# Kernel optimization log

Hardware: AMD Instinct MI355X
Metric: run time of the kernel (lower is better)

The kernel has to match this reference:

```python
import jax, jax.numpy as jnp
import numpy as np

NUM_HEADS = 8
SCALE = 3
TOPKS = [16, 8, 8]  # index 0 = coarsest level


def avg_pool2(t):
    B, C, H, W = t.shape
    return t.reshape(B, C, H // 2, 2, W // 2, 2).mean(axis=(3, 5))


def _to_heads(t, Hi, Wi):
    # [B, C, Hi, Wi] with C = nh*hd (head-major channels) -> [B, nh, Hi*Wi, hd]
    B, C = t.shape[0], t.shape[1]
    hd = C // NUM_HEADS
    return t.reshape(B, NUM_HEADS, hd, Hi * Wi).transpose(0, 1, 3, 2)


def setup_inputs() -> dict:
    key = jax.random.key(0)
    ks = jax.random.split(key, 6)
    B, H, W, C = 2, 96, 96, 128
    N = H * W
    s = 0.02
    return {
        "x": jax.random.normal(ks[0], (B, N, C), jnp.float32),
        "target": jax.random.normal(ks[1], (B, N, C), jnp.float32),
        "Wq": jax.random.normal(ks[2], (C, C), jnp.float32) * s,
        "Wk": jax.random.normal(ks[3], (C, C), jnp.float32) * s,
        "Wv": jax.random.normal(ks[4], (C, C), jnp.float32) * s,
        "Wo": jax.random.normal(ks[5], (C, C), jnp.float32) * s,
        "bo": jnp.zeros((C,), jnp.float32),
        "H": 96,
        "W": 96,
    }


def reference(x, target, Wq, Wk, Wv, Wo, bo, H, W):
    B, N, C = x.shape
    hd = C // NUM_HEADS
    temp = 1.0 / jnp.sqrt(jnp.float32(hd))
    xi = x.transpose(0, 2, 1).reshape(B, C, H, W)
    ti = target.transpose(0, 2, 1).reshape(B, C, H, W)
    # 1x1 conv projections == channel-wise matmul
    q = jnp.einsum('bchw,oc->bohw', xi, Wq)
    k = jnp.einsum('bchw,oc->bohw', ti, Wk)
    v = jnp.einsum('bchw,oc->bohw', ti, Wv)
    qs, ks_, vs, hw = [], [], [], []
    for i in range(SCALE):
        Hi, Wi = H >> i, W >> i
        qs.append(_to_heads(q, Hi, Wi))
        ks_.append(_to_heads(k, Hi, Wi))
        vs.append(_to_heads(v, Hi, Wi))
        hw.append((Hi, Wi))
        if i != SCALE - 1:
            q, k, v = avg_pool2(q), avg_pool2(k), avg_pool2(v)
    # ---- coarsest level: full attention + top-k key selection ----
    i = SCALE - 1
    A = jax.nn.softmax(temp * jnp.einsum('bhnd,bhmd->bhnm', qs[i], ks_[i]), axis=-1)
    msg = jnp.einsum('bhnm,bhmd->bhnd', A, vs[i])  # [B,h,Nc,hd]
    topk_score, topk_idx = jax.lax.top_k(A, TOPKS[0])  # [B,h,Nc,K]
    # ---- refine coarse -> fine over quadtree children of top-k keys ----
    gather = jax.vmap(jax.vmap(lambda arr, idx: arr[idx]))  # over B, h
    for lvl in range(SCALE - 2, -1, -1):
        Hi, Wi = hw[lvl]
        Hp, Wpar = hw[lvl + 1]
        Nf = Hi * Wi
        K = topk_idx.shape[-1]
        yf, xf = jnp.divmod(jnp.arange(Nf), Wi)
        parent = (yf // 2) * Wpar + (xf // 2)  # [Nf] parent query index
        p_idx = topk_idx[:, :, parent, :]  # [B,h,Nf,K] selected coarse keys
        ky, kx = jnp.divmod(p_idx, Wpar)
        dy = jnp.array([0, 0, 1, 1], jnp.int32)
        dx = jnp.array([0, 1, 0, 1], jnp.int32)
        child = ((2 * ky)[..., None] + dy) * Wi + (2 * kx)[..., None] + dx
        cand = child.reshape(B, NUM_HEADS, Nf, K * 4)  # candidate fine keys
        kg = gather(ks_[lvl], cand)  # [B,h,Nf,4K,hd]
        vg = gather(vs[lvl], cand)
        sc = temp * jnp.einsum('bhnd,bhnkd->bhnk', qs[lvl], kg)
        Af = jax.nn.softmax(sc, axis=-1)
        msg_f = jnp.einsum('bhnk,bhnkd->bhnd', Af, vg)
        msg = msg[:, :, parent, :] + msg_f  # assemble with upsampled coarse msg
        if lvl > 0:
            kk = TOPKS[SCALE - 1 - lvl]
            ts, tp = jax.lax.top_k(Af, kk)
            topk_idx = jnp.take_along_axis(cand, tp, axis=-1)
            topk_score = ts
    out = msg.transpose(0, 2, 1, 3).reshape(B, N, C)  # head-major channels
    return out @ Wo.T + bo
```

## Files before the change

kernel.cpp:

```cpp
#include <hip/hip_runtime.h>

#define NB   2
#define NHD  8
#define BH   16
#define HD   16
#define N0   9216
#define N1   2304
#define N2   576
#define W0_  96
#define W1_  48
#define W2_  24
#define M_TOT 18432
#define TEMP 0.25f

__global__ __launch_bounds__(256) void k_proj(const float* __restrict__ x, const float* __restrict__ tg,
    const float* __restrict__ Wq, const float* __restrict__ Wk, const float* __restrict__ Wv,
    float* __restrict__ q0, float* __restrict__ k0, float* __restrict__ v0)
{
    __shared__ __align__(16) float At[16][68];
    __shared__ __align__(16) float Wt[16][132];
    const int t = threadIdx.x;
    const int which = blockIdx.y;
    const float* A  = (which==0)? x : tg;
    const float* Wm = (which==0)? Wq : (which==1? Wk : Wv);
    float* dst      = (which==0)? q0 : (which==1? k0 : v0);
    const int m0 = blockIdx.x * 64;
    const int tx = t & 15, ty = t >> 4;

    float acc[4][8];
#pragma unroll
    for(int i=0;i<4;i++)
#pragma unroll
        for(int j=0;j<8;j++) acc[i][j]=0.f;

    const int ar = t>>2, akq = (t&3)*4;
    const int wo = t>>1, wkq = (t&1)*8;

    for(int kc=0;kc<128;kc+=16){
        float4 av = *(const float4*)(A + (m0+ar)*128 + kc + akq);
        At[akq+0][ar] = av.x;
        At[akq+1][ar] = av.y;
        At[akq+2][ar] = av.z;
        At[akq+3][ar] = av.w;
        float4 w0 = *(const float4*)(Wm + wo*128 + kc + wkq);
        float4 w1 = *(const float4*)(Wm + wo*128 + kc + wkq + 4);
        Wt[wkq+0][wo] = w0.x; Wt[wkq+1][wo] = w0.y;
        Wt[wkq+2][wo] = w0.z; Wt[wkq+3][wo] = w0.w;
        Wt[wkq+4][wo] = w1.x; Wt[wkq+5][wo] = w1.y;
        Wt[wkq+6][wo] = w1.z; Wt[wkq+7][wo] = w1.w;
        __syncthreads();
#pragma unroll
        for(int kk=0;kk<16;kk++){
            float4 a4 = *(const float4*)&At[kk][ty*4];
            float4 wa = *(const float4*)&Wt[kk][tx*4];
            float4 wb = *(const float4*)&Wt[kk][64 + tx*4];
            float avr[4] = {a4.x,a4.y,a4.z,a4.w};
            float wvr[8] = {wa.x,wa.y,wa.z,wa.w, wb.x,wb.y,wb.z,wb.w};
#pragma unroll
            for(int i=0;i<4;i++)
#pragma unroll
                for(int j=0;j<8;j++) acc[i][j] += avr[i]*wvr[j];
        }
        __syncthreads();
    }
    const int hA = tx>>2, dA = (tx&3)*4;
#pragma unroll
    for(int i=0;i<4;i++){
        int m = m0 + ty*4 + i;
        int b = m / N0; int n = m - b*N0;
        float4 sA = make_float4(acc[i][0], acc[i][1], acc[i][2], acc[i][3]);
        float4 sB = make_float4(acc[i][4], acc[i][5], acc[i][6], acc[i][7]);
        *(float4*)(dst + ((b*NHD + hA    )*N0 + n)*16 + dA) = sA;
        *(float4*)(dst + ((b*NHD + hA + 4)*N0 + n)*16 + dA) = sB;
    }
}

__global__ __launch_bounds__(256) void k_pool01(const float4* __restrict__ src0,
    float4* __restrict__ dst1, float4* __restrict__ q2f,
    float4* __restrict__ k2T, float4* __restrict__ v2T)
{
    int tid = blockIdx.x*256 + threadIdx.x;
    if (tid >= 110592) return;
    int d4 = tid & 3;
    int rest = tid >> 2;
    int n2 = rest % N2; int g = rest / N2;
    int yo2 = n2 / W2_, xo2 = n2 - yo2*W2_;

    const float4* s = src0 + g*N0*4;
    float4* d1 = dst1 + g*N1*4;
    float4 l1[4];
#pragma unroll
    for(int yy=0;yy<2;yy++){
#pragma unroll
        for(int xx=0;xx<2;xx++){
            int y1 = 2*yo2+yy, x1 = 2*xo2+xx;
            int n1 = y1*W1_ + x1;
            int cbase = (2*y1)*W0_ + 2*x1;
            float4 a = s[(cbase       )*4 + d4];
            float4 b = s[(cbase+1     )*4 + d4];
            float4 c = s[(cbase+W0_   )*4 + d4];
            float4 d = s[(cbase+W0_+1 )*4 + d4];
            float4 o;
            o.x = 0.25f*(a.x+b.x+c.x+d.x);
            o.y = 0.25f*(a.y+b.y+c.y+d.y);
            o.z = 0.25f*(a.z+b.z+c.z+d.z);
            o.w = 0.25f*(a.w+b.w+c.w+d.w);
            d1[n1*4 + d4] = o;
            l1[yy*2+xx] = o;
        }
    }
    float4 o2;
    o2.x = 0.25f*(l1[0].x+l1[1].x+l1[2].x+l1[3].x);
    o2.y = 0.25f*(l1[0].y+l1[1].y+l1[2].y+l1[3].y);
    o2.z = 0.25f*(l1[0].z+l1[1].z+l1[2].z+l1[3].z);
    o2.w = 0.25f*(l1[0].w+l1[1].w+l1[2].w+l1[3].w);
    int grp = g >> 4, bh = g & 15;
    if (grp == 0)      q2f[(bh*N2 + n2)*4 + d4] = o2;
    else if (grp == 1) k2T[(bh*4 + d4)*N2 + n2] = o2;
    else               v2T[(bh*4 + d4)*N2 + n2] = o2;
}

__global__ __launch_bounds__(256) void k_attn2(const float* __restrict__ q2, const float* __restrict__ k2,
    const float* __restrict__ v2, float* __restrict__ msg2, int* __restrict__ idx2)
{
    __shared__ __align__(16) float cval[4][580];
    __shared__ __align__(16) int   cidx[4][580];
    const int bh = blockIdx.x;
    const int wv = threadIdx.x>>6, lane = threadIdx.x&63;
    const int q = blockIdx.y*4 + wv;

    float qr[16];
    const float4* qp = (const float4*)(q2 + (bh*N2 + q)*16);
#pragma unroll
    for(int dq=0;dq<4;dq++){
        float4 va = qp[dq];
        qr[dq*4+0]=va.x; qr[dq*4+1]=va.y; qr[dq*4+2]=va.z; qr[dq*4+3]=va.w;
    }

    const float4* kT = (const float4*)k2 + bh*4*N2;
    const float4* vT = (const float4*)v2 + bh*4*N2;

    float ev[9];
    float mx = -1e30f;
#pragma unroll
    for(int t9=0;t9<9;t9++){
        int m = t9*64 + lane;
        float s = 0.f;
#pragma unroll
        for(int dg=0;dg<4;dg++){
            float4 kv = kT[dg*N2 + m];
            s += qr[dg*4+0]*kv.x;
            s += qr[dg*4+1]*kv.y;
            s += qr[dg*4+2]*kv.z;
            s += qr[dg*4+3]*kv.w;
        }
        s *= TEMP;
        ev[t9]=s;
        mx = fmaxf(mx, s);
    }
#pragma unroll
    for(int st=1; st<64; st<<=1) mx = fmaxf(mx, __shfl_xor(mx, st));

    float sum=0.f;
    float acc[16];
#pragma unroll
    for(int d=0;d<16;d++) acc[d]=0.f;
#pragma unroll
    for(int t9=0;t9<9;t9++){
        int m = t9*64 + lane;
        float e = expf(ev[t9]-mx);
        ev[t9]=e;
        sum += e;
#pragma unroll
        for(int dg=0;dg<4;dg++){
            float4 vv = vT[dg*N2 + m];
            acc[dg*4+0] += e*vv.x;
            acc[dg*4+1] += e*vv.y;
            acc[dg*4+2] += e*vv.z;
            acc[dg*4+3] += e*vv.w;
        }
    }
#pragma unroll
    for(int st=1; st<64; st<<=1) sum += __shfl_xor(sum, st);

    const bool b5 = (lane & 32) != 0;
    float r8[8];
#pragma unroll
    for(int i=0;i<8;i++){
        float snd  = b5 ? acc[i]   : acc[i+8];
        float kept = b5 ? acc[i+8] : acc[i];
        r8[i] = kept + __shfl_xor(snd, 32);
    }
    const bool b4 = (lane & 16) != 0;
    float r4[4];
#pragma unroll
    for(int i=0;i<4;i++){
        float snd  = b4 ? r8[i]   : r8[i+4];
        float kept = b4 ? r8[i+4] : r8[i];
        r4[i] = kept + __shfl_xor(snd, 16);
    }
    const bool b3 = (lane & 8) != 0;
    float r2[2];
#pragma unroll
    for(int i=0;i<2;i++){
        float snd  = b3 ? r4[i]   : r4[i+2];
        float kept = b3 ? r4[i+2] : r4[i];
        r2[i] = kept + __shfl_xor(snd, 8);
    }
    const bool b2 = (lane & 4) != 0;
    {
        float snd  = b2 ? r2[0] : r2[1];
        float kept = b2 ? r2[1] : r2[0];
        r2[0] = kept + __shfl_xor(snd, 4);
    }
    r2[0] += __shfl_xor(r2[0], 2);
    r2[0] += __shfl_xor(r2[0], 1);

    float inv = 1.0f/sum;
    if ((lane&3)==0){
        msg2[(bh*N2+q)*16 + (lane>>2)] = r2[0]*inv;
    }

    float head = ev[0];
#pragma unroll
    for(int i=1;i<9;i++) head = fmaxf(head, ev[i]);

    float bv = head;
#pragma unroll
    for(int k=2;k<=64;k<<=1){
#pragma unroll
        for(int j=k>>1;j>=1;j>>=1){
            float pv = __shfl_xor(bv, j);
            bool keepmin = (((lane & k)==0) == ((lane & j)==0));
            bv = keepmin ? fminf(bv,pv) : fmaxf(bv,pv);
        }
    }
    float T = __shfl(bv, 48);

    int ci = 0;
#pragma unroll
    for(int i=0;i<9;i++) ci += (ev[i] >= T) ? 1 : 0;
    int ps = ci;
#pragma unroll
    for(int d=1;d<64;d<<=1){
        int t = __shfl_up(ps, d);
        if (lane >= d) ps += t;
    }
    int excl = ps - ci;
    int C = __shfl(ps, 63);

    float* cv = cval[wv];
    int*   cx = cidx[wv];
    int o = excl;
#pragma unroll
    for(int i=0;i<9;i++){
        if (ev[i] >= T){
            cv[o] = ev[i];
            cx[o] = i*64 + lane;
            o++;
        }
    }
    if (lane < 4){ cv[C+lane] = -1.0f; cx[C+lane] = 0x7fffffff; }

    int* ip = idx2 + (bh*N2+q)*16;
    for(int l=lane; l<C; l+=64){
        float mv = cv[l]; int mi = cx[l];
        int rank = 0;
        for(int c=0;c<C;c+=4){
            float4 vv = *(const float4*)(cv + c);
            int4   ii = *(const int4*)(cx + c);
            rank += (vv.x > mv || (vv.x == mv && ii.x < mi)) ? 1 : 0;
            rank += (vv.y > mv || (vv.y == mv && ii.y < mi)) ? 1 : 0;
            rank += (vv.z > mv || (vv.z == mv && ii.z < mi)) ? 1 : 0;
            rank += (vv.w > mv || (vv.w == mv && ii.w < mi)) ? 1 : 0;
        }
        if (rank < 16) ip[rank] = mi;
    }
}

__global__ __launch_bounds__(256) void k_ref10(
    const float* __restrict__ q1, const float* __restrict__ k1, const float* __restrict__ v1,
    const float* __restrict__ q0, const float* __restrict__ k0, const float* __restrict__ v0,
    const float* __restrict__ msg2, const int* __restrict__ idx2, float* __restrict__ msg0)
{
    __shared__ float msg1s[4][16];
    __shared__ int   idx1s[4][8];
    const int bid = (blockIdx.x & 7)*1152 + (blockIdx.x >> 3);
    const int bh = bid / 576, tile = bid - bh*576;
    const int tyy = tile / 24, txx = tile - tyy*24;
    const int py0 = tyy*2, px0 = txx*2;
    const int wv = threadIdx.x>>6, lane = threadIdx.x&63;

    const int ppy = py0 + (wv>>1), ppx = px0 + (wv&1);

    {
        const int n  = ppy*W1_ + ppx;
        const int par = (ppy>>1)*W2_ + (ppx>>1);
        const int kk = lane>>2, tt = lane&3, dy = tt>>1, dx = tt&1;
        int p = idx2[(bh*N2+par)*16 + kk];
        int ky = p / W2_, kx = p - ky*W2_;
        int child = (2*ky+dy)*W1_ + 2*kx+dx;

        const float* qp = q1 + (bh*N1+n)*16;
        float qr[16];
#pragma unroll
        for(int d=0; d<16; d+=4){
            float4 qq = *(const float4*)(qp+d);
            qr[d]=qq.x; qr[d+1]=qq.y; qr[d+2]=qq.z; qr[d+3]=qq.w;
        }
        const float4* kp = (const float4*)(k1 + (bh*N1+child)*16);
        float s = 0.f;
#pragma unroll
        for(int dq=0;dq<4;dq++){
            float4 kv = kp[dq];
            s += qr[dq*4+0]*kv.x + qr[dq*4+1]*kv.y + qr[dq*4+2]*kv.z + qr[dq*4+3]*kv.w;
        }
        s *= TEMP;
        float e = expf(s);
        float sum = e;
#pragma unroll
        for(int st=1; st<64; st<<=1) sum += __shfl_xor(sum, st);

        float acc[16];
        const float4* vp = (const float4*)(v1 + (bh*N1+child)*16);
#pragma unroll
        for(int dq=0;dq<4;dq++){
            float4 vv = vp[dq];
            acc[dq*4+0]=e*vv.x; acc[dq*4+1]=e*vv.y; acc[dq*4+2]=e*vv.z; acc[dq*4+3]=e*vv.w;
        }
        const bool b5 = (lane & 32) != 0;
        float r8[8];
#pragma unroll
        for(int ii=0;ii<8;ii++){
            float snd  = b5 ? acc[ii]   : acc[ii+8];
            float kept = b5 ? acc[ii+8] : acc[ii];
            r8[ii] = kept + __shfl_xor(snd, 32);
        }
        const bool b4 = (lane & 16) != 0;
        float r4[4];
#pragma unroll
        for(int ii=0;ii<4;ii++){
            float snd  = b4 ? r8[ii]   : r8[ii+4];
            float kept = b4 ? r8[ii+4] : r8[ii];
            r4[ii] = kept + __shfl_xor(snd, 16);
        }
        const bool b3 = (lane & 8) != 0;
        float r2[2];
#pragma unroll
        for(int ii=0;ii<2;ii++){
            float snd  = b3 ? r4[ii]   : r4[ii+2];
            float kept = b3 ? r4[ii+2] : r4[ii];
            r2[ii] = kept + __shfl_xor(snd, 8);
        }
        const bool b2 = (lane & 4) != 0;
        {
            float snd  = b2 ? r2[0] : r2[1];
            float kept = b2 ? r2[1] : r2[0];
            r2[0] = kept + __shfl_xor(snd, 4);
        }
        r2[0] += __shfl_xor(r2[0], 2);
        r2[0] += __shfl_xor(r2[0], 1);

        float inv1 = 1.0f/sum;
        if ((lane&3)==0){
            int d = lane>>2;
            msg1s[wv][d] = msg2[(bh*N2+par)*16 + d] + r2[0]*inv1;
        }
        int cnt = 0;
#pragma unroll
        for(int ii=0;ii<64;ii++){
            float si = __shfl(s, ii);
            if (si > s || (si == s && ii < lane)) cnt++;
        }
        if (cnt < 8) idx1s[wv][cnt] = child;
    }

    const int j = lane & 31, sub = lane >> 5;
    const int kk = j>>2, tt = j&3, dy = tt>>1, dx = tt&1;
    int p = idx1s[wv][kk];
    int ky = p / W1_, kx = p - ky*W1_;
    int child = (2*ky+dy)*W0_ + 2*kx+dx;

    float kr[16];
    {
        const float4* kp = (const float4*)(k0 + (bh*N0+child)*16);
#pragma unroll
        for(int dq=0;dq<4;dq++){
            float4 kv = kp[dq];
            kr[dq*4+0]=kv.x; kr[dq*4+1]=kv.y; kr[dq*4+2]=kv.z; kr[dq*4+3]=kv.w;
        }
    }
    const int cy0 = 2*ppy, cx0 = 2*ppx + sub;
    int nq[2];
    float s_[2];
#pragma unroll
    for(int it=0; it<2; it++){
        nq[it] = (cy0+it)*W0_ + cx0;
        const float* qp = q0 + (bh*N0+nq[it])*16;
        float qr[16];
#pragma unroll
        for(int d=0; d<16; d+=4){
            float4 qq = *(const float4*)(qp+d);
            qr[d]=qq.x; qr[d+1]=qq.y; qr[d+2]=qq.z; qr[d+3]=qq.w;
        }
        float s = 0.f;
#pragma unroll
        for(int dq=0;dq<4;dq++){
            s += qr[dq*4+0]*kr[dq*4+0] + qr[dq*4+1]*kr[dq*4+1]
               + qr[dq*4+2]*kr[dq*4+2] + qr[dq*4+3]*kr[dq*4+3];
        }
        s_[it] = s * TEMP;
    }
    float vr[16];
    {
        const float4* vp = (const float4*)(v0 + (bh*N0+child)*16);
#pragma unroll
        for(int dq=0;dq<4;dq++){
            float4 vv = vp[dq];
            vr[dq*4+0]=vv.x; vr[dq*4+1]=vv.y; vr[dq*4+2]=vv.z; vr[dq*4+3]=vv.w;
        }
    }
    const float m1d = msg1s[wv][j>>1];

#pragma unroll
    for(int it=0; it<2; it++){
        float e = expf(s_[it]);
        float sum = e;
#pragma unroll
        for(int st=1; st<32; st<<=1) sum += __shfl_xor(sum, st);

        float acc[16];
#pragma unroll
        for(int d=0;d<16;d++) acc[d] = e*vr[d];

        const bool b4 = (j & 16) != 0;
        float r8[8];
#pragma unroll
        for(int ii=0;ii<8;ii++){
            float snd  = b4 ? acc[ii]   : acc[ii+8];
            float kept = b4 ? acc[ii+8] : acc[ii];
            r8[ii] = kept + __shfl_xor(snd, 16);
        }
        const bool b3 = (j & 8) != 0;
        float r4[4];
#pragma unroll
        for(int ii=0;ii<4;ii++){
            float snd  = b3 ? r8[ii]   : r8[ii+4];
            float kept = b3 ? r8[ii+4] : r8[ii];
            r4[ii] = kept + __shfl_xor(snd, 8);
        }
        const bool b2 = (j & 4) != 0;
        float r2[2];
#pragma unroll
        for(int ii=0;ii<2;ii++){
            float snd  = b2 ? r4[ii]   : r4[ii+2];
            float kept = b2 ? r4[ii+2] : r4[ii];
            r2[ii] = kept + __shfl_xor(snd, 4);
        }
        const bool b1 = (j & 2) != 0;
        {
            float snd  = b1 ? r2[0] : r2[1];
            float kept = b1 ? r2[1] : r2[0];
            r2[0] = kept + __shfl_xor(snd, 2);
        }
        r2[0] += __shfl_xor(r2[0], 1);

        float inv = 1.0f/sum;
        if ((j&1)==0){
            int d = j>>1;
            int b_ = bh>>3, h = bh&7;
            msg0[(b_*N0+nq[it])*128 + h*16 + d] = m1d + r2[0]*inv;
        }
    }
}

__global__ __launch_bounds__(256) void k_out(const float* __restrict__ msg0, const float* __restrict__ Wo,
    const float* __restrict__ bo, float* __restrict__ out)
{
    __shared__ __align__(16) float At[16][68];
    __shared__ __align__(16) float Wt[16][132];
    const int t = threadIdx.x;
    const int m0 = blockIdx.x * 64;
    const int tx = t & 15, ty = t >> 4;

    float acc[4][8];
#pragma unroll
    for(int i=0;i<4;i++)
#pragma unroll
        for(int j=0;j<8;j++) acc[i][j]=0.f;

    const int ar = t>>2, akq = (t&3)*4;
    const int wo = t>>1, wkq = (t&1)*8;

    for(int kc=0;kc<128;kc+=16){
        float4 av = *(const float4*)(msg0 + (m0+ar)*128 + kc + akq);
        At[akq+0][ar] = av.x;
        At[akq+1][ar] = av.y;
        At[akq+2][ar] = av.z;
        At[akq+3][ar] = av.w;
        float4 w0 = *(const float4*)(Wo + wo*128 + kc + wkq);
        float4 w1 = *(const float4*)(Wo + wo*128 + kc + wkq + 4);
        Wt[wkq+0][wo] = w0.x; Wt[wkq+1][wo] = w0.y;
        Wt[wkq+2][wo] = w0.z; Wt[wkq+3][wo] = w0.w;
        Wt[wkq+4][wo] = w1.x; Wt[wkq+5][wo] = w1.y;
        Wt[wkq+6][wo] = w1.z; Wt[wkq+7][wo] = w1.w;
        __syncthreads();
#pragma unroll
        for(int kk=0;kk<16;kk++){
            float4 a4 = *(const float4*)&At[kk][ty*4];
            float4 wa = *(const float4*)&Wt[kk][tx*4];
            float4 wb = *(const float4*)&Wt[kk][64 + tx*4];
            float avr[4] = {a4.x,a4.y,a4.z,a4.w};
            float wvr[8] = {wa.x,wa.y,wa.z,wa.w, wb.x,wb.y,wb.z,wb.w};
#pragma unroll
            for(int i=0;i<4;i++)
#pragma unroll
                for(int j=0;j<8;j++) acc[i][j] += avr[i]*wvr[j];
        }
        __syncthreads();
    }
#pragma unroll
    for(int i=0;i<4;i++){
        int m = m0 + ty*4 + i;
        float4 sA = make_float4(acc[i][0]+bo[tx*4+0], acc[i][1]+bo[tx*4+1],
                                acc[i][2]+bo[tx*4+2], acc[i][3]+bo[tx*4+3]);
        float4 sB = make_float4(acc[i][4]+bo[64+tx*4+0], acc[i][5]+bo[64+tx*4+1],
                                acc[i][6]+bo[64+tx*4+2], acc[i][7]+bo[64+tx*4+3]);
        *(float4*)(out + m*128 + tx*4)      = sA;
        *(float4*)(out + m*128 + 64 + tx*4) = sB;
    }
}

extern "C" void kernel_launch(void* const* d_in, const int* in_sizes, int n_in,
                              void* d_out, int out_size, void* d_ws, size_t ws_size,
                              hipStream_t stream) {
    const float* x  = (const float*)d_in[0];
    const float* tg = (const float*)d_in[1];
    const float* Wq = (const float*)d_in[2];
    const float* Wk = (const float*)d_in[3];
    const float* Wv = (const float*)d_in[4];
    const float* Wo = (const float*)d_in[5];
    const float* bo = (const float*)d_in[6];

    float* ws = (float*)d_ws;
    float* q0   = ws + 0;
    float* k0   = ws + 2359296;
    float* v0   = ws + 4718592;
    float* q1   = ws + 7077888;
    float* k1   = ws + 7667712;
    float* v1   = ws + 8257536;
    float* q2   = ws + 8847360;
    float* k2   = ws + 8994816;
    float* v2   = ws + 9142272;
    float* msg2 = ws + 9289728;
    float* msg0 = ws + 10027008;
    int*   idx2 = (int*)(ws + 12386304);

    k_proj<<<dim3(288,3), 256, 0, stream>>>(x, tg, Wq, Wk, Wv, q0, k0, v0);
    k_pool01<<<432, 256, 0, stream>>>((const float4*)q0, (float4*)q1,
                                      (float4*)q2, (float4*)k2, (float4*)v2);
    k_attn2<<<dim3(16,144), 256, 0, stream>>>(q2, k2, v2, msg2, idx2);
    k_ref10<<<9216, 256, 0, stream>>>(q1, k1, v1, q0, k0, v0, msg2, idx2, msg0);
    k_out<<<288, 256, 0, stream>>>(msg0, Wo, bo, (float*)d_out);
}
```

Baseline: 218.1 us.

## Process two queries per wave in coarse attention; bitonic+ballot top-8 in refine

The coarse attention kernel now has each wavefront handle two queries, so every loaded key and value vector is reused twice. The grid is halved to match, and the top-16 selection is moved into a shared helper that runs once per query. In the level-1 refine kernel, the 64-step shuffle rank count for top-8 is replaced by a bitonic sort to find the threshold, followed by ballot and mbcnt to assign slots. This lowers global loads and shuffle count, at the cost of more registers per thread in the attention kernel.

Result: faster. 206.7 us (-5.2%).

```diff
diff --git a/kernel.cpp b/kernel.cpp
--- a/kernel.cpp
+++ b/kernel.cpp
@@ -120,107 +120,8 @@
     else               v2T[(bh*4 + d4)*N2 + n2] = o2;
 }
 
-__global__ __launch_bounds__(256) void k_attn2(const float* __restrict__ q2, const float* __restrict__ k2,
-    const float* __restrict__ v2, float* __restrict__ msg2, int* __restrict__ idx2)
+__device__ __forceinline__ void top16_sel(const float ev[9], int lane, float* cv, int* cx, int* ip)
 {
-    __shared__ __align__(16) float cval[4][580];
-    __shared__ __align__(16) int   cidx[4][580];
-    const int bh = blockIdx.x;
-    const int wv = threadIdx.x>>6, lane = threadIdx.x&63;
-    const int q = blockIdx.y*4 + wv;
-
-    float qr[16];
-    const float4* qp = (const float4*)(q2 + (bh*N2 + q)*16);
-#pragma unroll
-    for(int dq=0;dq<4;dq++){
-        float4 va = qp[dq];
-        qr[dq*4+0]=va.x; qr[dq*4+1]=va.y; qr[dq*4+2]=va.z; qr[dq*4+3]=va.w;
-    }
-
-    const float4* kT = (const float4*)k2 + bh*4*N2;
-    const float4* vT = (const float4*)v2 + bh*4*N2;
-
-    float ev[9];
-    float mx = -1e30f;
-#pragma unroll
-    for(int t9=0;t9<9;t9++){
-        int m = t9*64 + lane;
-        float s = 0.f;
-#pragma unroll
-        for(int dg=0;dg<4;dg++){
-            float4 kv = kT[dg*N2 + m];
-            s += qr[dg*4+0]*kv.x;
-            s += qr[dg*4+1]*kv.y;
-            s += qr[dg*4+2]*kv.z;
-            s += qr[dg*4+3]*kv.w;
-        }
-        s *= TEMP;
-        ev[t9]=s;
-        mx = fmaxf(mx, s);
-    }
-#pragma unroll
-    for(int st=1; st<64; st<<=1) mx = fmaxf(mx, __shfl_xor(mx, st));
-
-    float sum=0.f;
-    float acc[16];
-#pragma unroll
-    for(int d=0;d<16;d++) acc[d]=0.f;
-#pragma unroll
-    for(int t9=0;t9<9;t9++){
-        int m = t9*64 + lane;
-        float e = expf(ev[t9]-mx);
-        ev[t9]=e;
-        sum += e;
-#pragma unroll
-        for(int dg=0;dg<4;dg++){
-            float4 vv = vT[dg*N2 + m];
-            acc[dg*4+0] += e*vv.x;
-            acc[dg*4+1] += e*vv.y;
-            acc[dg*4+2] += e*vv.z;
-            acc[dg*4+3] += e*vv.w;
-        }
-    }
-#pragma unroll
-    for(int st=1; st<64; st<<=1) sum += __shfl_xor(sum, st);
-
-    const bool b5 = (lane & 32) != 0;
-    float r8[8];
-#pragma unroll
-    for(int i=0;i<8;i++){
-        float snd  = b5 ? acc[i]   : acc[i+8];
-        float kept = b5 ? acc[i+8] : acc[i];
-        r8[i] = kept + __shfl_xor(snd, 32);
-    }
-    const bool b4 = (lane & 16) != 0;
-    float r4[4];
-#pragma unroll
-    for(int i=0;i<4;i++){
-        float snd  = b4 ? r8[i]   : r8[i+4];
-        float kept = b4 ? r8[i+4] : r8[i];
-        r4[i] = kept + __shfl_xor(snd, 16);
-    }
-    const bool b3 = (lane & 8) != 0;
-    float r2[2];
-#pragma unroll
-    for(int i=0;i<2;i++){
-        float snd  = b3 ? r4[i]   : r4[i+2];
-        float kept = b3 ? r4[i+2] : r4[i];
-        r2[i] = kept + __shfl_xor(snd, 8);
-    }
-    const bool b2 = (lane & 4) != 0;
-    {
-        float snd  = b2 ? r2[0] : r2[1];
-        float kept = b2 ? r2[1] : r2[0];
-        r2[0] = kept + __shfl_xor(snd, 4);
-    }
-    r2[0] += __shfl_xor(r2[0], 2);
-    r2[0] += __shfl_xor(r2[0], 1);
-
-    float inv = 1.0f/sum;
-    if ((lane&3)==0){
-        msg2[(bh*N2+q)*16 + (lane>>2)] = r2[0]*inv;
-    }
-
     float head = ev[0];
 #pragma unroll
     for(int i=1;i<9;i++) head = fmaxf(head, ev[i]);
@@ -249,8 +150,6 @@
     int excl = ps - ci;
     int C = __shfl(ps, 63);
 
-    float* cv = cval[wv];
-    int*   cx = cidx[wv];
     int o = excl;
 #pragma unroll
     for(int i=0;i<9;i++){
@@ -262,7 +161,6 @@
     }
     if (lane < 4){ cv[C+lane] = -1.0f; cx[C+lane] = 0x7fffffff; }
 
-    int* ip = idx2 + (bh*N2+q)*16;
     for(int l=lane; l<C; l+=64){
         float mv = cv[l]; int mi = cx[l];
         int rank = 0;
@@ -276,6 +174,128 @@
         }
         if (rank < 16) ip[rank] = mi;
     }
+}
+
+__global__ __launch_bounds__(256) void k_attn2(const float* __restrict__ q2, const float* __restrict__ k2,
+    const float* __restrict__ v2, float* __restrict__ msg2, int* __restrict__ idx2)
+{
+    __shared__ __align__(16) float cval[4][580];
+    __shared__ __align__(16) int   cidx[4][580];
+    const int bh = blockIdx.x;
+    const int wv = threadIdx.x>>6, lane = threadIdx.x&63;
+    const int qA = blockIdx.y*8 + wv*2;
+    const int qB = qA + 1;
+
+    float qrA[16], qrB[16];
+    {
+        const float4* qpA = (const float4*)(q2 + (bh*N2 + qA)*16);
+        const float4* qpB = (const float4*)(q2 + (bh*N2 + qB)*16);
+#pragma unroll
+        for(int dq=0;dq<4;dq++){
+            float4 va = qpA[dq];
+            qrA[dq*4+0]=va.x; qrA[dq*4+1]=va.y; qrA[dq*4+2]=va.z; qrA[dq*4+3]=va.w;
+            float4 vb = qpB[dq];
+            qrB[dq*4+0]=vb.x; qrB[dq*4+1]=vb.y; qrB[dq*4+2]=vb.z; qrB[dq*4+3]=vb.w;
+        }
+    }
+
+    const float4* kT = (const float4*)k2 + bh*4*N2;
+    const float4* vT = (const float4*)v2 + bh*4*N2;
+
+    float evA[9], evB[9];
+    float mxA = -1e30f, mxB = -1e30f;
+#pragma unroll
+    for(int t9=0;t9<9;t9++){
+        int m = t9*64 + lane;
+        float sA = 0.f, sB = 0.f;
+#pragma unroll
+        for(int dg=0;dg<4;dg++){
+            float4 kv = kT[dg*N2 + m];
+            sA += qrA[dg*4+0]*kv.x + qrA[dg*4+1]*kv.y + qrA[dg*4+2]*kv.z + qrA[dg*4+3]*kv.w;
+            sB += qrB[dg*4+0]*kv.x + qrB[dg*4+1]*kv.y + qrB[dg*4+2]*kv.z + qrB[dg*4+3]*kv.w;
+        }
+        sA *= TEMP; sB *= TEMP;
+        evA[t9]=sA; evB[t9]=sB;
+        mxA = fmaxf(mxA, sA);
+        mxB = fmaxf(mxB, sB);
+    }
+#pragma unroll
+    for(int st=1; st<64; st<<=1){
+        mxA = fmaxf(mxA, __shfl_xor(mxA, st));
+        mxB = fmaxf(mxB, __shfl_xor(mxB, st));
+    }
+
+    float sumA=0.f, sumB=0.f;
+    float accA[16], accB[16];
+#pragma unroll
+    for(int d=0;d<16;d++){ accA[d]=0.f; accB[d]=0.f; }
+#pragma unroll
+    for(int t9=0;t9<9;t9++){
+        int m = t9*64 + lane;
+        float eA = expf(evA[t9]-mxA);
+        float eB = expf(evB[t9]-mxB);
+        evA[t9]=eA; evB[t9]=eB;
+        sumA += eA; sumB += eB;
+#pragma unroll
+        for(int dg=0;dg<4;dg++){
+            float4 vv = vT[dg*N2 + m];
+            accA[dg*4+0] += eA*vv.x; accA[dg*4+1] += eA*vv.y;
+            accA[dg*4+2] += eA*vv.z; accA[dg*4+3] += eA*vv.w;
+            accB[dg*4+0] += eB*vv.x; accB[dg*4+1] += eB*vv.y;
+            accB[dg*4+2] += eB*vv.z; accB[dg*4+3] += eB*vv.w;
+        }
+    }
+#pragma unroll
+    for(int st=1; st<64; st<<=1){
+        sumA += __shfl_xor(sumA, st);
+        sumB += __shfl_xor(sumB, st);
+    }
+
+    const bool b5 = (lane & 32) != 0;
+    const bool b4 = (lane & 16) != 0;
+    const bool b3 = (lane & 8) != 0;
+    const bool b2 = (lane & 4) != 0;
+#pragma unroll
+    for(int which=0; which<2; which++){
+        float* acc = which ? accB : accA;
+        float sum  = which ? sumB : sumA;
+        int   q    = which ? qB   : qA;
+        float r8[8];
+#pragma unroll
+        for(int i=0;i<8;i++){
+            float snd  = b5 ? acc[i]   : acc[i+8];
+            float kept = b5 ? acc[i+8] : acc[i];
+            r8[i] = kept + __shfl_xor(snd, 32);
+        }
+        float r4[4];
+#pragma unroll
+        for(int i=0;i<4;i++){
+            float snd  = b4 ? r8[i]   : r8[i+4];
+            float kept = b4 ? r8[i+4] : r8[i];
+            r4[i] = kept + __shfl_xor(snd, 16);
+        }
+        float r2[2];
+#pragma unroll
+        for(int i=0;i<2;i++){
+            float snd  = b3 ? r4[i]   : r4[i+2];
+            float kept = b3 ? r4[i+2] : r4[i];
+            r2[i] = kept + __shfl_xor(snd, 8);
+        }
+        {
+            float snd  = b2 ? r2[0] : r2[1];
+            float kept = b2 ? r2[1] : r2[0];
+            r2[0] = kept + __shfl_xor(snd, 4);
+        }
+        r2[0] += __shfl_xor(r2[0], 2);
+        r2[0] += __shfl_xor(r2[0], 1);
+        float inv = 1.0f/sum;
+        if ((lane&3)==0){
+            msg2[(bh*N2+q)*16 + (lane>>2)] = r2[0]*inv;
+        }
+    }
+
+    top16_sel(evA, lane, cval[wv], cidx[wv], idx2 + (bh*N2+qA)*16);
+    top16_sel(evB, lane, cval[wv], cidx[wv], idx2 + (bh*N2+qB)*16);
 }
 
 __global__ __launch_bounds__(256) void k_ref10(
@@ -366,13 +386,27 @@
             int d = lane>>2;
             msg1s[wv][d] = msg2[(bh*N2+par)*16 + d] + r2[0]*inv1;
         }
-        int cnt = 0;
-#pragma unroll
-        for(int ii=0;ii<64;ii++){
-            float si = __shfl(s, ii);
-            if (si > s || (si == s && ii < lane)) cnt++;
-        }
-        if (cnt < 8) idx1s[wv][cnt] = child;
+
+        float bv = s;
+#pragma unroll
+        for(int kb=2;kb<=64;kb<<=1){
+#pragma unroll
+            for(int jb=kb>>1;jb>=1;jb>>=1){
+                float pv = __shfl_xor(bv, jb);
+                bool keepmin = (((lane & kb)==0) == ((lane & jb)==0));
+                bv = keepmin ? fminf(bv,pv) : fmaxf(bv,pv);
+            }
+        }
+        float T8 = __shfl(bv, 56);
+        unsigned long long mgt = __ballot(s > T8);
+        unsigned long long meq = __ballot(s == T8);
+        int ngt = (int)__popcll(mgt);
+        int ltg = __builtin_amdgcn_mbcnt_lo((unsigned)mgt, 0);
+        ltg = __builtin_amdgcn_mbcnt_hi((unsigned)(mgt>>32), ltg);
+        int lte = __builtin_amdgcn_mbcnt_lo((unsigned)meq, 0);
+        lte = __builtin_amdgcn_mbcnt_hi((unsigned)(meq>>32), lte);
+        int slot = (s > T8) ? ltg : ((s == T8) ? (ngt + lte) : 8);
+        if (slot < 8) idx1s[wv][slot] = child;
     }
 
     const int j = lane & 31, sub = lane >> 5;
@@ -559,7 +593,7 @@
     k_proj<<<dim3(288,3), 256, 0, stream>>>(x, tg, Wq, Wk, Wv, q0, k0, v0);
     k_pool01<<<432, 256, 0, stream>>>((const float4*)q0, (float4*)q1,
                                       (float4*)q2, (float4*)k2, (float4*)v2);
-    k_attn2<<<dim3(16,144), 256, 0, stream>>>(q2, k2, v2, msg2, idx2);
+    k_attn2<<<dim3(16,72), 256, 0, stream>>>(q2, k2, v2, msg2, idx2);
     k_ref10<<<9216, 256, 0, stream>>>(q1, k1, v1, q0, k0, v0, msg2, idx2, msg0);
     k_out<<<288, 256, 0, stream>>>(msg0, Wo, bo, (float*)d_out);
 }
```
